# Kernel tuning notes

Measured on AMD Instinct MI355X. Metric: run time of the kernel, lower is better.

Reference implementation:

```python
import jax, jax.numpy as jnp
import numpy as np

D_MODEL = 1024
N_HEADS = 16
DH = (D_MODEL // N_HEADS) // 2  # depth // 2 = 32
B, S = 4, 2048


def setup_inputs() -> dict:
    key = jax.random.key(0)
    ks = jax.random.split(key, 8)
    scale_in = 1.0
    q = jax.random.normal(ks[0], (B, S, D_MODEL), dtype=jnp.float32)
    k = jax.random.normal(ks[1], (B, S, D_MODEL), dtype=jnp.float32)
    v = jax.random.normal(ks[2], (B, S, D_MODEL), dtype=jnp.float32)
    # Per-head projection weights stacked over the head axis (glorot-ish init)
    w_std = (2.0 / (D_MODEL + DH)) ** 0.5
    Wq = jax.random.normal(ks[3], (N_HEADS, D_MODEL, DH), dtype=jnp.float32) * w_std
    Wk = jax.random.normal(ks[4], (N_HEADS, D_MODEL, DH), dtype=jnp.float32) * w_std
    Wv = jax.random.normal(ks[5], (N_HEADS, D_MODEL, DH), dtype=jnp.float32) * w_std
    wo_std = (2.0 / (N_HEADS * DH + D_MODEL)) ** 0.5
    Wo = jax.random.normal(ks[6], (N_HEADS * DH, D_MODEL), dtype=jnp.float32) * wo_std
    return {"q": q, "k": k, "v": v, "Wq": Wq, "Wk": Wk, "Wv": Wv, "Wo": Wo}


def reference(q, k, v, Wq, Wk, Wv, Wo):
    # NOTE: source scales by d_model**-0.5 (not head_dim**-0.5)
    scale = D_MODEL ** (-0.5)
    Q = jnp.einsum("bsd,hde->bhse", q, Wq)   # [B,H,S,DH]
    K = jnp.einsum("btd,hde->bhte", k, Wk)
    V = jnp.einsum("btd,hde->bhte", v, Wv)
    attn = jnp.einsum("bhse,bhte->bhst", Q, K) * scale  # [B,H,S,S]
    attn = jax.nn.softmax(attn, axis=-1)
    x = jnp.einsum("bhst,bhte->bhse", attn, V)  # [B,H,S,DH]
    # concat heads along feature dim (head order = concat order in source)
    x = jnp.transpose(x, (0, 2, 1, 3)).reshape(q.shape[0], q.shape[1], N_HEADS * DH)
    return x @ Wo  # [B,S,D_MODEL]; dropout is identity (training=False)
```

## Files before the change

### kernel.cpp

```cpp
#include <hip/hip_runtime.h>
#include <hip/hip_bf16.h>

typedef __attribute__((ext_vector_type(8))) short short8;
typedef __attribute__((ext_vector_type(4))) float f32x4;
typedef __attribute__((ext_vector_type(4))) float fv4;
typedef __attribute__((ext_vector_type(4))) unsigned int u32x4;

#define MFMA16(a, b, c) __builtin_amdgcn_mfma_f32_16x16x32_bf16((a), (b), (c), 0, 0, 0)
#define SBAR() __builtin_amdgcn_sched_barrier(0)
#define RBAR() __builtin_amdgcn_s_barrier()

typedef const __attribute__((address_space(1))) unsigned int gu32;
typedef __attribute__((address_space(3))) unsigned int lu32;

__device__ __forceinline__ short f2b(float f) {
  unsigned int x = __builtin_bit_cast(unsigned int, f);
  x += 0x7fffu + ((x >> 16) & 1u);
  return (short)(x >> 16);
}

__device__ __forceinline__ unsigned int cvtpk(float lo, float hi) {
  unsigned int r;
  asm("v_cvt_pk_bf16_f32 %0, %1, %2" : "=v"(r) : "v"(lo), "v"(hi));
  return r;
}

#define hexp2(x) __builtin_amdgcn_exp2f(x)

__global__ void prep_weights(const float* __restrict__ Wq, const float* __restrict__ Wk,
                             const float* __restrict__ Wv, const float* __restrict__ Wo,
                             short* __restrict__ WqT, short* __restrict__ WkT,
                             short* __restrict__ WvT, short* __restrict__ WoT) {
  const float SC2 = 0.045084220027780106f;
  int idx = blockIdx.x * 256 + threadIdx.x;
  if (idx < 3 * 512 * 1024) {
    int wsel = idx >> 19;
    int rem = idx & ((1 << 19) - 1);
    int n = rem >> 10;
    int d = rem & 1023;
    const float* W = (wsel == 0) ? Wq : ((wsel == 1) ? Wk : Wv);
    short* WT = (wsel == 0) ? WqT : ((wsel == 1) ? WkT : WvT);
    float v = W[(n >> 5) * (1024 * 32) + d * 32 + (n & 31)];
    if (wsel == 0) v *= SC2;
    WT[n * 1024 + d] = f2b(v);
  } else {
    int idx2 = idx - 3 * 512 * 1024;
    int n = idx2 >> 9;
    int kk = idx2 & 511;
    WoT[n * 512 + kk] = f2b(Wo[kk * 1024 + n]);
  }
}

__global__ __launch_bounds__(256, 3) void proj_gemm(
    const float* __restrict__ q, const float* __restrict__ k, const float* __restrict__ v,
    const short* __restrict__ BTall,
    short* __restrict__ Qb, short* __restrict__ Kb, short* __restrict__ Vtb) {
  __shared__ char smem[49152];
  const int tid = threadIdx.x;
  const int lane = tid & 63;
  const int w = tid >> 6;
  const int l15 = lane & 15, g = lane >> 4;
  const int wm = (w >> 1) * 64, wn = (w & 1) * 64;
  const int id = blockIdx.x;
  const int bm = id & 63;
  const int bn = id >> 6;
  const int bm0 = bm * 128, bn0 = bn * 128;
  const int z = blockIdx.y;
  (void)z;
  const float* A = q;
  (void)A;

  const int zz = bn >> 2;
  const int bnz = bn & 3;
  const float* Az = (zz == 0) ? q : ((zz == 1) ? k : v);
  const short* BT = BTall + (size_t)zz * 512 * 1024;
  const int bn0z = bnz * 128;

  const int ar = (lane >> 3);
  const int au = lane & 7;
  const int br = (lane >> 2);
  const int bu = lane & 3;

  f32x4 zf = {0.f, 0.f, 0.f, 0.f};
  f32x4 acc[4][4];
#pragma unroll
  for (int a = 0; a < 4; ++a)
#pragma unroll
    for (int bq = 0; bq < 4; ++bq) acc[a][bq] = zf;

#define STAGE(base, k0)                                                        \
  {                                                                            \
    _Pragma("unroll") for (int i = 0; i < 4; ++i) {                            \
      int row = 32 * w + 8 * i + ar;                                           \
      __builtin_amdgcn_global_load_lds(                                        \
          (gu32*)(Az + (size_t)(bm0 + row) * 1024 + (k0) + 4 * (au ^ (row & 7))), \
          (lu32*)(smem + (base) + w * 4096 + i * 1024), 16, 0, 0);             \
    }                                                                          \
    _Pragma("unroll") for (int i = 0; i < 2; ++i) {                            \
      int row = 32 * w + 16 * i + br;                                          \
      __builtin_amdgcn_global_load_lds(                                        \
          (gu32*)(BT + (size_t)(bn0z + row) * 1024 + (k0) +                    \
                  8 * (bu ^ ((row >> 1) & 3))),                                \
          (lu32*)(smem + (base) + 16384 + w * 2048 + i * 1024), 16, 0, 0);     \
    }                                                                          \
  }

#define COMPUTE(base)                                                          \
  {                                                                            \
    short8 af[4], bfr[4];                                                      \
    _Pragma("unroll") for (int mf = 0; mf < 4; ++mf) {                         \
      int row = wm + mf * 16 + l15;                                            \
      fv4 a0 = *(const fv4*)(smem + (base) + row * 128 +                       \
                             (((2 * g) ^ (row & 7)) * 16));                    \
      fv4 a1 = *(const fv4*)(smem + (base) + row * 128 +                       \
                             (((2 * g + 1) ^ (row & 7)) * 16));                \
      u32x4 wv;                                                                \
      wv[0] = cvtpk(a0[0], a0[1]);                                             \
      wv[1] = cvtpk(a0[2], a0[3]);                                             \
      wv[2] = cvtpk(a1[0], a1[1]);                                             \
      wv[3] = cvtpk(a1[2], a1[3]);                                             \
      af[mf] = __builtin_bit_cast(short8, wv);                                 \
    }                                                                          \
    _Pragma("unroll") for (int nf = 0; nf < 4; ++nf) {                         \
      int row = wn + nf * 16 + l15;                                            \
      bfr[nf] = *(const short8*)(smem + (base) + 16384 + row * 64 +            \
                                 ((g ^ ((row >> 1) & 3)) * 16));               \
    }                                                                          \
    _Pragma("unroll") for (int mf = 0; mf < 4; ++mf)                           \
        _Pragma("unroll") for (int nf = 0; nf < 4; ++nf)                       \
            acc[mf][nf] = MFMA16(af[mf], bfr[nf], acc[mf][nf]);                \
  }

  STAGE(0, 0);
  for (int k0 = 0; k0 < 1024; k0 += 32) {
    const int cur = (k0 >> 5) & 1;
    const int cbase = cur * 24576;
    const int nbase = (cur ^ 1) * 24576;
    if (k0 + 32 < 1024) {
      STAGE(nbase, k0 + 32);
      asm volatile("s_waitcnt vmcnt(6)" ::: "memory");
    } else {
      asm volatile("s_waitcnt vmcnt(0)" ::: "memory");
    }
    RBAR();
    SBAR();
    COMPUTE(cbase);
    RBAR();
  }
#undef STAGE
#undef COMPUTE

#pragma unroll
  for (int mf = 0; mf < 4; ++mf)
#pragma unroll
    for (int nf = 0; nf < 4; ++nf)
#pragma unroll
      for (int i = 0; i < 4; ++i) {
        int row = bm0 + wm + mf * 16 + g * 4 + i;
        int col = bn0z + wn + nf * 16 + l15;
        int bb = row >> 11, ss = row & 2047;
        int hh = col >> 5, ee = col & 31;
        short val = f2b(acc[mf][nf][i]);
        if (zz == 2)
          Vtb[((size_t)(bb * 16 + hh) * 32 + ee) * 2048 + ss] = val;
        else if (zz == 1)
          Kb[((size_t)(bb * 16 + hh) * 2048 + ss) * 32 + ee] = val;
        else
          Qb[((size_t)(bb * 16 + hh) * 2048 + ss) * 32 + ee] = val;
      }
}

__global__ __launch_bounds__(256, 2) void out_gemm(const short* __restrict__ X,
                                                   const short* __restrict__ WoT,
                                                   float* __restrict__ out) {
  __shared__ char smem[32768];
  const int tid = threadIdx.x;
  const int lane = tid & 63;
  const int w = tid >> 6;
  const int l15 = lane & 15, g = lane >> 4;
  const int wm = (w >> 1) * 64, wn = (w & 1) * 64;
  const int id = blockIdx.x;
  const int bm0 = (id & 63) * 128, bn0 = (id >> 6) * 128;

  const int br = (lane >> 2);
  const int bu = lane & 3;

  f32x4 zf = {0.f, 0.f, 0.f, 0.f};
  f32x4 acc[4][4];
#pragma unroll
  for (int a = 0; a < 4; ++a)
#pragma unroll
    for (int bq = 0; bq < 4; ++bq) acc[a][bq] = zf;

#define STAGE(base, k0)                                                        \
  {                                                                            \
    _Pragma("unroll") for (int i = 0; i < 2; ++i) {                            \
      int row = 32 * w + 16 * i + br;                                          \
      __builtin_amdgcn_global_load_lds(                                        \
          (gu32*)(X + (size_t)(bm0 + row) * 512 + (k0) +                       \
                  8 * (bu ^ ((row >> 1) & 3))),                                \
          (lu32*)(smem + (base) + w * 2048 + i * 1024), 16, 0, 0);             \
      __builtin_amdgcn_global_load_lds(                                        \
          (gu32*)(WoT + (size_t)(bn0 + row) * 512 + (k0) +                     \
                  8 * (bu ^ ((row >> 1) & 3))),                                \
          (lu32*)(smem + (base) + 8192 + w * 2048 + i * 1024), 16, 0, 0);      \
    }                                                                          \
  }

#define COMPUTE(base)                                                          \
  {                                                                            \
    short8 af[4], bfr[4];                                                      \
    _Pragma("unroll") for (int mf = 0; mf < 4; ++mf) {                         \
      int row = wm + mf * 16 + l15;                                            \
      af[mf] = *(const short8*)(smem + (base) + row * 64 +                     \
                                ((g ^ ((row >> 1) & 3)) * 16));                \
    }                                                                          \
    _Pragma("unroll") for (int nf = 0; nf < 4; ++nf) {                         \
      int row = wn + nf * 16 + l15;                                            \
      bfr[nf] = *(const short8*)(smem + (base) + 8192 + row * 64 +             \
                                 ((g ^ ((row >> 1) & 3)) * 16));               \
    }                                                                          \
    _Pragma("unroll") for (int mf = 0; mf < 4; ++mf)                           \
        _Pragma("unroll") for (int nf = 0; nf < 4; ++nf)                       \
            acc[mf][nf] = MFMA16(af[mf], bfr[nf], acc[mf][nf]);                \
  }

  STAGE(0, 0);
  for (int k0 = 0; k0 < 512; k0 += 32) {
    const int cur = (k0 >> 5) & 1;
    const int cbase = cur * 16384;
    const int nbase = (cur ^ 1) * 16384;
    if (k0 + 32 < 512) {
      STAGE(nbase, k0 + 32);
      asm volatile("s_waitcnt vmcnt(4)" ::: "memory");
    } else {
      asm volatile("s_waitcnt vmcnt(0)" ::: "memory");
    }
    RBAR();
    SBAR();
    COMPUTE(cbase);
    RBAR();
  }
#undef STAGE
#undef COMPUTE

#pragma unroll
  for (int mf = 0; mf < 4; ++mf)
#pragma unroll
    for (int nf = 0; nf < 4; ++nf)
#pragma unroll
      for (int i = 0; i < 4; ++i) {
        int row = bm0 + wm + mf * 16 + g * 4 + i;
        int col = bn0 + wn + nf * 16 + l15;
        out[(size_t)row * 1024 + col] = acc[mf][nf][i];
      }
}

__device__ __forceinline__ void qk_half(short8 k0, short8 k1, short8 k2, short8 k3,
                                        short8 qf, const f32x4& zf,
                                        short8& pf0, short8& pf1) {
  f32x4 s0 = MFMA16(k0, qf, zf);
  f32x4 s1 = MFMA16(k1, qf, zf);
  f32x4 s2 = MFMA16(k2, qf, zf);
  f32x4 s3 = MFMA16(k3, qf, zf);
#pragma unroll
  for (int i = 0; i < 4; ++i) {
    s0[i] = hexp2(s0[i]);
    s1[i] = hexp2(s1[i]);
    s2[i] = hexp2(s2[i]);
    s3[i] = hexp2(s3[i]);
  }
  u32x4 w0, w1;
  w0[0] = cvtpk(s0[0], s0[1]);
  w0[1] = cvtpk(s0[2], s0[3]);
  w0[2] = cvtpk(s1[0], s1[1]);
  w0[3] = cvtpk(s1[2], s1[3]);
  w1[0] = cvtpk(s2[0], s2[1]);
  w1[1] = cvtpk(s2[2], s2[3]);
  w1[2] = cvtpk(s3[0], s3[1]);
  w1[3] = cvtpk(s3[2], s3[3]);
  pf0 = __builtin_bit_cast(short8, w0);
  pf1 = __builtin_bit_cast(short8, w1);
}

__global__ __launch_bounds__(256, 4) void attn(const short* __restrict__ Qb,
                                               const short* __restrict__ Kb,
                                               const short* __restrict__ Vtb,
                                               short* __restrict__ X) {
  __shared__ short KV[2][2][2048];
  const int tid = threadIdx.x;
  const int lane = tid & 63;
  const int w = tid >> 6;
  const int l15 = lane & 15, g = lane >> 4;
  const int id = blockIdx.x;
  const int bh = id & 63;
  const int qblk = id >> 6;
  const int bb = bh >> 4, hh = bh & 15;
  const int q0 = qblk * 128 + w * 32;

  const short* Qp = Qb + ((size_t)bh * 2048 + q0) * 32;
  const short* Kp = Kb + (size_t)bh * 2048 * 32;
  const short* Vp = Vtb + (size_t)bh * 32 * 2048;

  short8 qfA = *(const short8*)(Qp + l15 * 32 + g * 8);
  short8 qfB = *(const short8*)(Qp + (16 + l15) * 32 + g * 8);

  const int kbase = 8 * (l15 >> 2) + (l15 & 3);
  const int koff = (w & 1) * 4 + (w >> 1) * 32;
  const int vrow = (w >> 1) * 16;
  const int vcol = (w & 1) * 32;
  const short* Ksrc0 = Kp + (size_t)(kbase + koff) * 32 + g * 8;
  const short* Vsrc0 = Vp + (size_t)(l15 + vrow) * 2048 + vcol + g * 8;

  f32x4 zf = {0.f, 0.f, 0.f, 0.f};
  f32x4 o_loA = zf, o_hiA = zf, o_loB = zf, o_hiB = zf;
  f32x4 accLA = zf, accLB = zf;
  u32x4 ones_u = {0x3F803F80u, 0x3F803F80u, 0x3F803F80u, 0x3F803F80u};
  const short8 ones = __builtin_bit_cast(short8, ones_u);

#define STAGE(b, t0)                                                        \
  {                                                                         \
    __builtin_amdgcn_global_load_lds((gu32*)(Ksrc0 + (size_t)(t0) * 32),    \
                                     (lu32*)&KV[b][0][w * 512], 16, 0, 0);  \
    __builtin_amdgcn_global_load_lds((gu32*)(Vsrc0 + (t0)),                 \
                                     (lu32*)&KV[b][1][w * 512], 16, 0, 0);  \
  }

#define BODY(b)                                                       \
  {                                                                   \
    short8 k0 = *(const short8*)(&KV[b][0][0 * 512 + lane * 8]);      \
    short8 k1 = *(const short8*)(&KV[b][0][1 * 512 + lane * 8]);      \
    short8 k2 = *(const short8*)(&KV[b][0][2 * 512 + lane * 8]);      \
    short8 k3 = *(const short8*)(&KV[b][0][3 * 512 + lane * 8]);      \
    short8 vlo0 = *(const short8*)(&KV[b][1][0 * 512 + lane * 8]);    \
    short8 vlo1 = *(const short8*)(&KV[b][1][1 * 512 + lane * 8]);    \
    short8 vhi0 = *(const short8*)(&KV[b][1][2 * 512 + lane * 8]);    \
    short8 vhi1 = *(const short8*)(&KV[b][1][3 * 512 + lane * 8]);    \
    short8 pfA0, pfA1, pfB0, pfB1;                                    \
    qk_half(k0, k1, k2, k3, qfA, zf, pfA0, pfA1);                     \
    qk_half(k0, k1, k2, k3, qfB, zf, pfB0, pfB1);                     \
    __builtin_amdgcn_s_setprio(1);                                    \
    accLA = MFMA16(pfA0, ones, accLA);                                \
    accLA = MFMA16(pfA1, ones, accLA);                                \
    accLB = MFMA16(pfB0, ones, accLB);                                \
    accLB = MFMA16(pfB1, ones, accLB);                                \
    o_loA = MFMA16(pfA0, vlo0, o_loA);                                \
    o_loA = MFMA16(pfA1, vlo1, o_loA);                                \
    o_hiA = MFMA16(pfA0, vhi0, o_hiA);                                \
    o_hiA = MFMA16(pfA1, vhi1, o_hiA);                                \
    o_loB = MFMA16(pfB0, vlo0, o_loB);                                \
    o_loB = MFMA16(pfB1, vlo1, o_loB);                                \
    o_hiB = MFMA16(pfB0, vhi0, o_hiB);                                \
    o_hiB = MFMA16(pfB1, vhi1, o_hiB);                                \
    __builtin_amdgcn_s_setprio(0);                                    \
  }

  STAGE(0, 0);
  __syncthreads();
  for (int t0 = 0; t0 < 2048; t0 += 128) {
    STAGE(1, t0 + 64);
    BODY(0);
    __syncthreads();
    if (t0 + 128 < 2048) {
      STAGE(0, t0 + 128);
    }
    BODY(1);
    __syncthreads();
  }
#undef STAGE
#undef BODY

#pragma unroll
  for (int i = 0; i < 4; ++i) {
    float invA = 1.0f / accLA[i];
    float invB = 1.0f / accLB[i];
    int ssA = q0 + 4 * g + i;
    size_t baseA = ((size_t)bb * 2048 + ssA) * 512 + hh * 32;
    X[baseA + l15] = f2b(o_loA[i] * invA);
    X[baseA + 16 + l15] = f2b(o_hiA[i] * invA);
    size_t baseB = baseA + (size_t)16 * 512;
    X[baseB + l15] = f2b(o_loB[i] * invB);
    X[baseB + 16 + l15] = f2b(o_hiB[i] * invB);
  }
}

extern "C" void kernel_launch(void* const* d_in, const int* in_sizes, int n_in,
                              void* d_out, int out_size, void* d_ws, size_t ws_size,
                              hipStream_t stream) {
  const float* q = (const float*)d_in[0];
  const float* k = (const float*)d_in[1];
  const float* v = (const float*)d_in[2];
  const float* Wq = (const float*)d_in[3];
  const float* Wk = (const float*)d_in[4];
  const float* Wv = (const float*)d_in[5];
  const float* Wo = (const float*)d_in[6];

  char* ws = (char*)d_ws;
  const size_t MB = 1u << 20;
  short* WqT = (short*)(ws + 0 * MB);
  short* WkT = (short*)(ws + 1 * MB);
  short* WvT = (short*)(ws + 2 * MB);
  short* WoT = (short*)(ws + 3 * MB);
  short* Qb  = (short*)(ws + 4 * MB);
  short* Kb  = (short*)(ws + 12 * MB);
  short* Vtb = (short*)(ws + 20 * MB);
  short* Xb  = (short*)(ws + 28 * MB);

  prep_weights<<<8192, 256, 0, stream>>>(Wq, Wk, Wv, Wo, WqT, WkT, WvT, WoT);
  proj_gemm<<<768, 256, 0, stream>>>(q, k, v, WqT, Qb, Kb, Vtb);
  attn<<<1024, 256, 0, stream>>>(Qb, Kb, Vtb, Xb);
  out_gemm<<<512, 256, 0, stream>>>(Xb, WoT, (float*)d_out);
}
```

Baseline: 118.1 us.

## Convert fp32 activations to bf16 in registers before staging to LDS in projection GEMM

Instead of copying the fp32 A tile straight into LDS with global_load_lds and converting it on every fragment read, each thread loads fp32 A into registers, converts it to bf16 and writes a swizzled bf16 tile into LDS. This halves the LDS footprint per stage (32 KB total instead of 48 KB), which could allow more resident blocks, and turns the A fragment read into a single short8 load. The cost is register pressure and exposed global-load latency, since the A prefetch goes through VGPRs and needs explicit vmcnt/lgkmcnt waits before the barrier.

Result: no change. 118.7 us (+0.5%).

```diff
diff --git a/kernel.cpp b/kernel.cpp
--- a/kernel.cpp
+++ b/kernel.cpp
@@ -55,7 +55,7 @@
     const float* __restrict__ q, const float* __restrict__ k, const float* __restrict__ v,
     const short* __restrict__ BTall,
     short* __restrict__ Qb, short* __restrict__ Kb, short* __restrict__ Vtb) {
-  __shared__ char smem[49152];
+  __shared__ char smem[32768];
   const int tid = threadIdx.x;
   const int lane = tid & 63;
   const int w = tid >> 6;
@@ -64,22 +64,23 @@
   const int id = blockIdx.x;
   const int bm = id & 63;
   const int bn = id >> 6;
-  const int bm0 = bm * 128, bn0 = bn * 128;
-  const int z = blockIdx.y;
-  (void)z;
-  const float* A = q;
-  (void)A;
-
   const int zz = bn >> 2;
   const int bnz = bn & 3;
   const float* Az = (zz == 0) ? q : ((zz == 1) ? k : v);
   const short* BT = BTall + (size_t)zz * 512 * 1024;
-  const int bn0z = bnz * 128;
-
-  const int ar = (lane >> 3);
-  const int au = lane & 7;
-  const int br = (lane >> 2);
-  const int bu = lane & 3;
+  const int bm0 = bm * 128, bn0z = bnz * 128;
+
+  const int arow = 32 * w + (lane >> 1);
+  const int ahalf = lane & 1;
+  const float* Ag = Az + (size_t)(bm0 + arow) * 1024 + ahalf * 16;
+  const int aswz = (arow >> 1) & 3;
+  const int aw_off0 = arow * 64 + (((2 * ahalf) ^ aswz) * 16);
+  const int aw_off1 = arow * 64 + (((2 * ahalf + 1) ^ aswz) * 16);
+
+  const int brow0 = 32 * w + (lane >> 2);
+  const int brow1 = brow0 + 16;
+  const short* Bg0 = BT + (size_t)(bn0z + brow0) * 1024 + 8 * ((lane & 3) ^ ((brow0 >> 1) & 3));
+  const short* Bg1 = BT + (size_t)(bn0z + brow1) * 1024 + 8 * ((lane & 3) ^ ((brow1 >> 1) & 3));
 
   f32x4 zf = {0.f, 0.f, 0.f, 0.f};
   f32x4 acc[4][4];
@@ -88,42 +89,47 @@
 #pragma unroll
     for (int bq = 0; bq < 4; ++bq) acc[a][bq] = zf;
 
-#define STAGE(base, k0)                                                        \
-  {                                                                            \
-    _Pragma("unroll") for (int i = 0; i < 4; ++i) {                            \
-      int row = 32 * w + 8 * i + ar;                                           \
-      __builtin_amdgcn_global_load_lds(                                        \
-          (gu32*)(Az + (size_t)(bm0 + row) * 1024 + (k0) + 4 * (au ^ (row & 7))), \
-          (lu32*)(smem + (base) + w * 4096 + i * 1024), 16, 0, 0);             \
-    }                                                                          \
-    _Pragma("unroll") for (int i = 0; i < 2; ++i) {                            \
-      int row = 32 * w + 16 * i + br;                                          \
-      __builtin_amdgcn_global_load_lds(                                        \
-          (gu32*)(BT + (size_t)(bn0z + row) * 1024 + (k0) +                    \
-                  8 * (bu ^ ((row >> 1) & 3))),                                \
-          (lu32*)(smem + (base) + 16384 + w * 2048 + i * 1024), 16, 0, 0);     \
-    }                                                                          \
-  }
-
-#define COMPUTE(base)                                                          \
+  fv4 fa0, fa1, fa2, fa3;
+#define GLOADA(k0)                      \
+  fa0 = *(const fv4*)(Ag + (k0));       \
+  fa1 = *(const fv4*)(Ag + (k0) + 4);   \
+  fa2 = *(const fv4*)(Ag + (k0) + 8);   \
+  fa3 = *(const fv4*)(Ag + (k0) + 12);
+
+#define WRITEA(abase)                                                      \
+  {                                                                        \
+    u32x4 wv0, wv1;                                                        \
+    wv0[0] = cvtpk(fa0[0], fa0[1]);                                        \
+    wv0[1] = cvtpk(fa0[2], fa0[3]);                                        \
+    wv0[2] = cvtpk(fa1[0], fa1[1]);                                        \
+    wv0[3] = cvtpk(fa1[2], fa1[3]);                                        \
+    wv1[0] = cvtpk(fa2[0], fa2[1]);                                        \
+    wv1[1] = cvtpk(fa2[2], fa2[3]);                                        \
+    wv1[2] = cvtpk(fa3[0], fa3[1]);                                        \
+    wv1[3] = cvtpk(fa3[2], fa3[3]);                                        \
+    *(short8*)(smem + (abase) + aw_off0) = __builtin_bit_cast(short8, wv0); \
+    *(short8*)(smem + (abase) + aw_off1) = __builtin_bit_cast(short8, wv1); \
+  }
+
+#define STAGEB(bbase, k0)                                                       \
+  {                                                                             \
+    __builtin_amdgcn_global_load_lds((gu32*)(Bg0 + (k0)),                       \
+                                     (lu32*)(smem + (bbase) + w * 2048), 16, 0, 0); \
+    __builtin_amdgcn_global_load_lds((gu32*)(Bg1 + (k0)),                       \
+                                     (lu32*)(smem + (bbase) + w * 2048 + 1024), 16, 0, 0); \
+  }
+
+#define COMPUTE(abase, bbase)                                                  \
   {                                                                            \
     short8 af[4], bfr[4];                                                      \
     _Pragma("unroll") for (int mf = 0; mf < 4; ++mf) {                         \
       int row = wm + mf * 16 + l15;                                            \
-      fv4 a0 = *(const fv4*)(smem + (base) + row * 128 +                       \
-                             (((2 * g) ^ (row & 7)) * 16));                    \
-      fv4 a1 = *(const fv4*)(smem + (base) + row * 128 +                       \
-                             (((2 * g + 1) ^ (row & 7)) * 16));                \
-      u32x4 wv;                                                                \
-      wv[0] = cvtpk(a0[0], a0[1]);                                             \
-      wv[1] = cvtpk(a0[2], a0[3]);                                             \
-      wv[2] = cvtpk(a1[0], a1[1]);                                             \
-      wv[3] = cvtpk(a1[2], a1[3]);                                             \
-      af[mf] = __builtin_bit_cast(short8, wv);                                 \
+      af[mf] = *(const short8*)(smem + (abase) + row * 64 +                    \
+                                ((g ^ ((row >> 1) & 3)) * 16));                \
     }                                                                          \
     _Pragma("unroll") for (int nf = 0; nf < 4; ++nf) {                         \
       int row = wn + nf * 16 + l15;                                            \
-      bfr[nf] = *(const short8*)(smem + (base) + 16384 + row * 64 +            \
+      bfr[nf] = *(const short8*)(smem + (bbase) + row * 64 +                   \
                                  ((g ^ ((row >> 1) & 3)) * 16));               \
     }                                                                          \
     _Pragma("unroll") for (int mf = 0; mf < 4; ++mf)                           \
@@ -131,23 +137,35 @@
             acc[mf][nf] = MFMA16(af[mf], bfr[nf], acc[mf][nf]);                \
   }
 
-  STAGE(0, 0);
+  GLOADA(0);
+  STAGEB(8192, 0);
+  SBAR();
+
   for (int k0 = 0; k0 < 1024; k0 += 32) {
     const int cur = (k0 >> 5) & 1;
-    const int cbase = cur * 24576;
-    const int nbase = (cur ^ 1) * 24576;
+    const int abase = cur * 16384;
+    const int bbase = cur * 16384 + 8192;
+    const int nabase = (cur ^ 1) * 16384;
+    (void)nabase;
+    SBAR();
+    WRITEA(abase);
     if (k0 + 32 < 1024) {
-      STAGE(nbase, k0 + 32);
-      asm volatile("s_waitcnt vmcnt(6)" ::: "memory");
+      GLOADA(k0 + 32);
+      STAGEB((cur ^ 1) * 16384 + 8192, k0 + 32);
+      SBAR();
+      asm volatile("s_waitcnt vmcnt(10)" ::: "memory");
     } else {
       asm volatile("s_waitcnt vmcnt(0)" ::: "memory");
     }
+    asm volatile("s_waitcnt lgkmcnt(0)" ::: "memory");
+    SBAR();
     RBAR();
-    SBAR();
-    COMPUTE(cbase);
+    COMPUTE(abase, bbase);
     RBAR();
   }
-#undef STAGE
+#undef GLOADA
+#undef WRITEA
+#undef STAGEB
 #undef COMPUTE
 
 #pragma unroll
```

## Enlarge projection GEMM tiles to 256x256 with 512-thread blocks and BK=64

Applied to the files above, without the earlier changes.

Restructures the QKV projection GEMM from 128x128 tiles with 256 threads and a double-buffered BK=32 loop to 256x256 tiles with 8 waves, BK=64 and a single LDS buffer. The aim is to halve how often each fp32 activation tile is re-read across the N dimension and to raise arithmetic per LDS load. In exchange, there is no prefetch overlap between global loads and MFMA work. The grid also drops to 192 blocks, fewer than the CU count, and 96 KB of LDS per block limits occupancy. The out_gemm sched_barrier is also removed.

Measured after the change: 143.2 us. 21.2% more time.

```diff
diff --git a/kernel.cpp b/kernel.cpp
--- a/kernel.cpp
+++ b/kernel.cpp
@@ -7,8 +7,6 @@
 typedef __attribute__((ext_vector_type(4))) unsigned int u32x4;
 
 #define MFMA16(a, b, c) __builtin_amdgcn_mfma_f32_16x16x32_bf16((a), (b), (c), 0, 0, 0)
-#define SBAR() __builtin_amdgcn_sched_barrier(0)
-#define RBAR() __builtin_amdgcn_s_barrier()
 
 typedef const __attribute__((address_space(1))) unsigned int gu32;
 typedef __attribute__((address_space(3))) unsigned int lu32;
@@ -51,113 +49,97 @@
   }
 }
 
-__global__ __launch_bounds__(256, 3) void proj_gemm(
+__global__ __launch_bounds__(512, 2) void proj_gemm(
     const float* __restrict__ q, const float* __restrict__ k, const float* __restrict__ v,
     const short* __restrict__ BTall,
     short* __restrict__ Qb, short* __restrict__ Kb, short* __restrict__ Vtb) {
-  __shared__ char smem[49152];
+  __shared__ char smem[98304];
   const int tid = threadIdx.x;
   const int lane = tid & 63;
   const int w = tid >> 6;
   const int l15 = lane & 15, g = lane >> 4;
-  const int wm = (w >> 1) * 64, wn = (w & 1) * 64;
+  const int wm = (w >> 2) * 128;
+  const int wn = (w & 3) * 64;
   const int id = blockIdx.x;
-  const int bm = id & 63;
-  const int bn = id >> 6;
-  const int bm0 = bm * 128, bn0 = bn * 128;
-  const int z = blockIdx.y;
-  (void)z;
-  const float* A = q;
-  (void)A;
-
-  const int zz = bn >> 2;
-  const int bnz = bn & 3;
+  const int mblk = id & 31;
+  const int nblk = id >> 5;
+  const int zz = nblk >> 1;
+  const int bnz = nblk & 1;
   const float* Az = (zz == 0) ? q : ((zz == 1) ? k : v);
   const short* BT = BTall + (size_t)zz * 512 * 1024;
-  const int bn0z = bnz * 128;
-
-  const int ar = (lane >> 3);
-  const int au = lane & 7;
-  const int br = (lane >> 2);
-  const int bu = lane & 3;
+  const int bm0 = mblk * 256;
+  const int bn0 = bnz * 256;
+
+  const int ar = lane >> 4;
+  const int as_ = lane & 15;
+  const int br_ = lane >> 3;
+  const int bs_ = lane & 7;
 
   f32x4 zf = {0.f, 0.f, 0.f, 0.f};
-  f32x4 acc[4][4];
-#pragma unroll
-  for (int a = 0; a < 4; ++a)
+  f32x4 acc[8][4];
+#pragma unroll
+  for (int a = 0; a < 8; ++a)
 #pragma unroll
     for (int bq = 0; bq < 4; ++bq) acc[a][bq] = zf;
 
-#define STAGE(base, k0)                                                        \
-  {                                                                            \
-    _Pragma("unroll") for (int i = 0; i < 4; ++i) {                            \
-      int row = 32 * w + 8 * i + ar;                                           \
-      __builtin_amdgcn_global_load_lds(                                        \
-          (gu32*)(Az + (size_t)(bm0 + row) * 1024 + (k0) + 4 * (au ^ (row & 7))), \
-          (lu32*)(smem + (base) + w * 4096 + i * 1024), 16, 0, 0);             \
-    }                                                                          \
-    _Pragma("unroll") for (int i = 0; i < 2; ++i) {                            \
-      int row = 32 * w + 16 * i + br;                                          \
-      __builtin_amdgcn_global_load_lds(                                        \
-          (gu32*)(BT + (size_t)(bn0z + row) * 1024 + (k0) +                    \
-                  8 * (bu ^ ((row >> 1) & 3))),                                \
-          (lu32*)(smem + (base) + 16384 + w * 2048 + i * 1024), 16, 0, 0);     \
-    }                                                                          \
-  }
-
-#define COMPUTE(base)                                                          \
-  {                                                                            \
-    short8 af[4], bfr[4];                                                      \
-    _Pragma("unroll") for (int mf = 0; mf < 4; ++mf) {                         \
-      int row = wm + mf * 16 + l15;                                            \
-      fv4 a0 = *(const fv4*)(smem + (base) + row * 128 +                       \
-                             (((2 * g) ^ (row & 7)) * 16));                    \
-      fv4 a1 = *(const fv4*)(smem + (base) + row * 128 +                       \
-                             (((2 * g + 1) ^ (row & 7)) * 16));                \
-      u32x4 wv;                                                                \
-      wv[0] = cvtpk(a0[0], a0[1]);                                             \
-      wv[1] = cvtpk(a0[2], a0[3]);                                             \
-      wv[2] = cvtpk(a1[0], a1[1]);                                             \
-      wv[3] = cvtpk(a1[2], a1[3]);                                             \
-      af[mf] = __builtin_bit_cast(short8, wv);                                 \
-    }                                                                          \
-    _Pragma("unroll") for (int nf = 0; nf < 4; ++nf) {                         \
-      int row = wn + nf * 16 + l15;                                            \
-      bfr[nf] = *(const short8*)(smem + (base) + 16384 + row * 64 +            \
-                                 ((g ^ ((row >> 1) & 3)) * 16));               \
-    }                                                                          \
-    _Pragma("unroll") for (int mf = 0; mf < 4; ++mf)                           \
-        _Pragma("unroll") for (int nf = 0; nf < 4; ++nf)                       \
-            acc[mf][nf] = MFMA16(af[mf], bfr[nf], acc[mf][nf]);                \
-  }
-
-  STAGE(0, 0);
-  for (int k0 = 0; k0 < 1024; k0 += 32) {
-    const int cur = (k0 >> 5) & 1;
-    const int cbase = cur * 24576;
-    const int nbase = (cur ^ 1) * 24576;
-    if (k0 + 32 < 1024) {
-      STAGE(nbase, k0 + 32);
-      asm volatile("s_waitcnt vmcnt(6)" ::: "memory");
-    } else {
-      asm volatile("s_waitcnt vmcnt(0)" ::: "memory");
-    }
-    RBAR();
-    SBAR();
-    COMPUTE(cbase);
-    RBAR();
-  }
-#undef STAGE
-#undef COMPUTE
-
-#pragma unroll
-  for (int mf = 0; mf < 4; ++mf)
+  for (int k0 = 0; k0 < 1024; k0 += 64) {
+#pragma unroll
+    for (int c = 0; c < 8; ++c) {
+      int row = 32 * w + 4 * c + ar;
+      int s = (as_ & 8) | ((as_ & 7) ^ (row & 7));
+      __builtin_amdgcn_global_load_lds(
+          (gu32*)(Az + (size_t)(bm0 + row) * 1024 + k0 + 4 * s),
+          (lu32*)(smem + w * 8192 + c * 1024), 16, 0, 0);
+    }
+#pragma unroll
+    for (int c = 0; c < 4; ++c) {
+      int row = 32 * w + 8 * c + br_;
+      int s = bs_ ^ (row & 7);
+      __builtin_amdgcn_global_load_lds(
+          (gu32*)(BT + (size_t)(bn0 + row) * 1024 + k0 + 8 * s),
+          (lu32*)(smem + 65536 + w * 4096 + c * 1024), 16, 0, 0);
+    }
+    __syncthreads();
+
+#pragma unroll
+    for (int kk = 0; kk < 2; ++kk) {
+      short8 bfr[4];
+#pragma unroll
+      for (int nf = 0; nf < 4; ++nf) {
+        int row = wn + nf * 16 + l15;
+        int s = (4 * kk + g) ^ (row & 7);
+        bfr[nf] = *(const short8*)(smem + 65536 + row * 128 + s * 16);
+      }
+#pragma unroll
+      for (int mf = 0; mf < 8; ++mf) {
+        int row = wm + mf * 16 + l15;
+        int s0 = 8 * kk + 2 * g;
+        int sa = (s0 & 8) | ((s0 & 7) ^ (row & 7));
+        int sb = ((s0 + 1) & 8) | (((s0 + 1) & 7) ^ (row & 7));
+        fv4 a0 = *(const fv4*)(smem + row * 256 + sa * 16);
+        fv4 a1 = *(const fv4*)(smem + row * 256 + sb * 16);
+        u32x4 wv;
+        wv[0] = cvtpk(a0[0], a0[1]);
+        wv[1] = cvtpk(a0[2], a0[3]);
+        wv[2] = cvtpk(a1[0], a1[1]);
+        wv[3] = cvtpk(a1[2], a1[3]);
+        short8 af = __builtin_bit_cast(short8, wv);
+#pragma unroll
+        for (int nf = 0; nf < 4; ++nf)
+          acc[mf][nf] = MFMA16(af, bfr[nf], acc[mf][nf]);
+      }
+    }
+    __syncthreads();
+  }
+
+#pragma unroll
+  for (int mf = 0; mf < 8; ++mf)
 #pragma unroll
     for (int nf = 0; nf < 4; ++nf)
 #pragma unroll
       for (int i = 0; i < 4; ++i) {
         int row = bm0 + wm + mf * 16 + g * 4 + i;
-        int col = bn0z + wn + nf * 16 + l15;
+        int col = bn0 + wn + nf * 16 + l15;
         int bb = row >> 11, ss = row & 2047;
         int hh = col >> 5, ee = col & 31;
         short val = f2b(acc[mf][nf][i]);
@@ -236,10 +218,9 @@
     } else {
       asm volatile("s_waitcnt vmcnt(0)" ::: "memory");
     }
-    RBAR();
-    SBAR();
+    __builtin_amdgcn_s_barrier();
     COMPUTE(cbase);
-    RBAR();
+    __builtin_amdgcn_s_barrier();
   }
 #undef STAGE
 #undef COMPUTE
@@ -407,7 +388,7 @@
   short* Xb  = (short*)(ws + 28 * MB);
 
   prep_weights<<<8192, 256, 0, stream>>>(Wq, Wk, Wv, Wo, WqT, WkT, WvT, WoT);
-  proj_gemm<<<768, 256, 0, stream>>>(q, k, v, WqT, Qb, Kb, Vtb);
+  proj_gemm<<<192, 512, 0, stream>>>(q, k, v, WqT, Qb, Kb, Vtb);
   attn<<<1024, 256, 0, stream>>>(Qb, Kb, Vtb, Xb);
   out_gemm<<<512, 256, 0, stream>>>(Xb, WoT, (float*)d_out);
 }
```

## Triple-buffer LDS pipelines in projection and output GEMMs with MFMA priority boost

Applied to the files above, without the earlier changes.

Both projection and output GEMMs move from double to triple buffering of LDS tiles, keeping two stages of global_load_lds in flight, with vmcnt waits adjusted and the main loop unrolled by three. s_setprio raises wave priority around the MFMA block, and B fragments are loaded before A conversions. The goal is to hide global memory latency better. The cost is more LDS per block, which lowers proj_gemm occupancy from 3 to 2 blocks per CU.

Result: slower. 122.6 us (+3.8%).

```diff
diff --git a/kernel.cpp b/kernel.cpp
--- a/kernel.cpp
+++ b/kernel.cpp
@@ -51,11 +51,11 @@
   }
 }
 
-__global__ __launch_bounds__(256, 3) void proj_gemm(
+__global__ __launch_bounds__(256, 2) void proj_gemm(
     const float* __restrict__ q, const float* __restrict__ k, const float* __restrict__ v,
     const short* __restrict__ BTall,
     short* __restrict__ Qb, short* __restrict__ Kb, short* __restrict__ Vtb) {
-  __shared__ char smem[49152];
+  __shared__ char smem[73728];
   const int tid = threadIdx.x;
   const int lane = tid & 63;
   const int w = tid >> 6;
@@ -64,21 +64,15 @@
   const int id = blockIdx.x;
   const int bm = id & 63;
   const int bn = id >> 6;
-  const int bm0 = bm * 128, bn0 = bn * 128;
-  const int z = blockIdx.y;
-  (void)z;
-  const float* A = q;
-  (void)A;
-
   const int zz = bn >> 2;
   const int bnz = bn & 3;
   const float* Az = (zz == 0) ? q : ((zz == 1) ? k : v);
   const short* BT = BTall + (size_t)zz * 512 * 1024;
-  const int bn0z = bnz * 128;
-
-  const int ar = (lane >> 3);
+  const int bm0 = bm * 128, bn0z = bnz * 128;
+
+  const int ar = lane >> 3;
   const int au = lane & 7;
-  const int br = (lane >> 2);
+  const int br = lane >> 2;
   const int bu = lane & 3;
 
   f32x4 zf = {0.f, 0.f, 0.f, 0.f};
@@ -88,26 +82,33 @@
 #pragma unroll
     for (int bq = 0; bq < 4; ++bq) acc[a][bq] = zf;
 
-#define STAGE(base, k0)                                                        \
-  {                                                                            \
-    _Pragma("unroll") for (int i = 0; i < 4; ++i) {                            \
-      int row = 32 * w + 8 * i + ar;                                           \
-      __builtin_amdgcn_global_load_lds(                                        \
-          (gu32*)(Az + (size_t)(bm0 + row) * 1024 + (k0) + 4 * (au ^ (row & 7))), \
-          (lu32*)(smem + (base) + w * 4096 + i * 1024), 16, 0, 0);             \
-    }                                                                          \
-    _Pragma("unroll") for (int i = 0; i < 2; ++i) {                            \
-      int row = 32 * w + 16 * i + br;                                          \
-      __builtin_amdgcn_global_load_lds(                                        \
-          (gu32*)(BT + (size_t)(bn0z + row) * 1024 + (k0) +                    \
-                  8 * (bu ^ ((row >> 1) & 3))),                                \
-          (lu32*)(smem + (base) + 16384 + w * 2048 + i * 1024), 16, 0, 0);     \
-    }                                                                          \
+#define STAGE(base, k0)                                                          \
+  {                                                                              \
+    _Pragma("unroll") for (int i = 0; i < 2; ++i) {                              \
+      int rowa = 32 * w + 8 * i + ar;                                            \
+      __builtin_amdgcn_global_load_lds(                                          \
+          (gu32*)(Az + (size_t)(bm0 + rowa) * 1024 + (k0) + 4 * (au ^ (rowa & 7))), \
+          (lu32*)(smem + (base) + w * 4096 + i * 1024), 16, 0, 0);               \
+      int rowa2 = 32 * w + 8 * (i + 2) + ar;                                     \
+      __builtin_amdgcn_global_load_lds(                                          \
+          (gu32*)(Az + (size_t)(bm0 + rowa2) * 1024 + (k0) + 4 * (au ^ (rowa2 & 7))), \
+          (lu32*)(smem + (base) + w * 4096 + (i + 2) * 1024), 16, 0, 0);         \
+      int rowb = 32 * w + 16 * i + br;                                           \
+      __builtin_amdgcn_global_load_lds(                                          \
+          (gu32*)(BT + (size_t)(bn0z + rowb) * 1024 + (k0) +                     \
+                  8 * (bu ^ ((rowb >> 1) & 3))),                                 \
+          (lu32*)(smem + (base) + 16384 + w * 2048 + i * 1024), 16, 0, 0);       \
+    }                                                                            \
   }
 
 #define COMPUTE(base)                                                          \
   {                                                                            \
     short8 af[4], bfr[4];                                                      \
+    _Pragma("unroll") for (int nf = 0; nf < 4; ++nf) {                         \
+      int row = wn + nf * 16 + l15;                                            \
+      bfr[nf] = *(const short8*)(smem + (base) + 16384 + row * 64 +            \
+                                 ((g ^ ((row >> 1) & 3)) * 16));               \
+    }                                                                          \
     _Pragma("unroll") for (int mf = 0; mf < 4; ++mf) {                         \
       int row = wm + mf * 16 + l15;                                            \
       fv4 a0 = *(const fv4*)(smem + (base) + row * 128 +                       \
@@ -121,34 +122,47 @@
       wv[3] = cvtpk(a1[2], a1[3]);                                             \
       af[mf] = __builtin_bit_cast(short8, wv);                                 \
     }                                                                          \
-    _Pragma("unroll") for (int nf = 0; nf < 4; ++nf) {                         \
-      int row = wn + nf * 16 + l15;                                            \
-      bfr[nf] = *(const short8*)(smem + (base) + 16384 + row * 64 +            \
-                                 ((g ^ ((row >> 1) & 3)) * 16));               \
-    }                                                                          \
+    __builtin_amdgcn_s_setprio(1);                                             \
     _Pragma("unroll") for (int mf = 0; mf < 4; ++mf)                           \
         _Pragma("unroll") for (int nf = 0; nf < 4; ++nf)                       \
             acc[mf][nf] = MFMA16(af[mf], bfr[nf], acc[mf][nf]);                \
+    __builtin_amdgcn_s_setprio(0);                                             \
+  }
+
+#define PBODY(s_, cb_, nb_)                                 \
+  {                                                         \
+    STAGE(nb_, ((s_) + 2) * 32);                            \
+    SBAR();                                                 \
+    asm volatile("s_waitcnt vmcnt(12)" ::: "memory");       \
+    SBAR();                                                 \
+    RBAR();                                                 \
+    COMPUTE(cb_);                                           \
+    RBAR();                                                 \
   }
 
   STAGE(0, 0);
-  for (int k0 = 0; k0 < 1024; k0 += 32) {
-    const int cur = (k0 >> 5) & 1;
-    const int cbase = cur * 24576;
-    const int nbase = (cur ^ 1) * 24576;
-    if (k0 + 32 < 1024) {
-      STAGE(nbase, k0 + 32);
-      asm volatile("s_waitcnt vmcnt(6)" ::: "memory");
-    } else {
-      asm volatile("s_waitcnt vmcnt(0)" ::: "memory");
-    }
-    RBAR();
-    SBAR();
-    COMPUTE(cbase);
-    RBAR();
-  }
+  STAGE(24576, 32);
+
+  for (int s = 0; s < 30; s += 3) {
+    PBODY(s, 0, 49152);
+    PBODY(s + 1, 24576, 0);
+    PBODY(s + 2, 49152, 24576);
+  }
+  SBAR();
+  asm volatile("s_waitcnt vmcnt(6)" ::: "memory");
+  SBAR();
+  RBAR();
+  COMPUTE(0);
+  RBAR();
+  SBAR();
+  asm volatile("s_waitcnt vmcnt(0)" ::: "memory");
+  SBAR();
+  RBAR();
+  COMPUTE(24576);
+  RBAR();
 #undef STAGE
 #undef COMPUTE
+#undef PBODY
 
 #pragma unroll
   for (int mf = 0; mf < 4; ++mf)
@@ -173,7 +187,7 @@
 __global__ __launch_bounds__(256, 2) void out_gemm(const short* __restrict__ X,
                                                    const short* __restrict__ WoT,
                                                    float* __restrict__ out) {
-  __shared__ char smem[32768];
+  __shared__ char smem[49152];
   const int tid = threadIdx.x;
   const int lane = tid & 63;
   const int w = tid >> 6;
@@ -182,7 +196,7 @@
   const int id = blockIdx.x;
   const int bm0 = (id & 63) * 128, bn0 = (id >> 6) * 128;
 
-  const int br = (lane >> 2);
+  const int br = lane >> 2;
   const int bu = lane & 3;
 
   f32x4 zf = {0.f, 0.f, 0.f, 0.f};
@@ -220,29 +234,48 @@
       bfr[nf] = *(const short8*)(smem + (base) + 8192 + row * 64 +             \
                                  ((g ^ ((row >> 1) & 3)) * 16));               \
     }                                                                          \
+    __builtin_amdgcn_s_setprio(1);                                             \
     _Pragma("unroll") for (int mf = 0; mf < 4; ++mf)                           \
         _Pragma("unroll") for (int nf = 0; nf < 4; ++nf)                       \
             acc[mf][nf] = MFMA16(af[mf], bfr[nf], acc[mf][nf]);                \
+    __builtin_amdgcn_s_setprio(0);                                             \
+  }
+
+#define PBODY(s_, cb_, nb_)                                 \
+  {                                                         \
+    STAGE(nb_, ((s_) + 2) * 32);                            \
+    SBAR();                                                 \
+    asm volatile("s_waitcnt vmcnt(8)" ::: "memory");        \
+    SBAR();                                                 \
+    RBAR();                                                 \
+    COMPUTE(cb_);                                           \
+    RBAR();                                                 \
   }
 
   STAGE(0, 0);
-  for (int k0 = 0; k0 < 512; k0 += 32) {
-    const int cur = (k0 >> 5) & 1;
-    const int cbase = cur * 16384;
-    const int nbase = (cur ^ 1) * 16384;
-    if (k0 + 32 < 512) {
-      STAGE(nbase, k0 + 32);
-      asm volatile("s_waitcnt vmcnt(4)" ::: "memory");
-    } else {
-      asm volatile("s_waitcnt vmcnt(0)" ::: "memory");
-    }
-    RBAR();
-    SBAR();
-    COMPUTE(cbase);
-    RBAR();
-  }
+  STAGE(16384, 32);
+  for (int s = 0; s < 12; s += 3) {
+    PBODY(s, 0, 32768);
+    PBODY(s + 1, 16384, 0);
+    PBODY(s + 2, 32768, 16384);
+  }
+  PBODY(12, 0, 32768);
+  PBODY(13, 16384, 0);
+  SBAR();
+  asm volatile("s_waitcnt vmcnt(4)" ::: "memory");
+  SBAR();
+  RBAR();
+  COMPUTE(32768);
+  RBAR();
+  SBAR();
+  asm volatile("s_waitcnt vmcnt(0)" ::: "memory");
+  SBAR();
+  RBAR();
+  COMPUTE(0);
+  RBAR();
 #undef STAGE
 #undef COMPUTE
+#undef PBODY
 
 #pragma unroll
   for (int mf = 0; mf < 4; ++mf)
```
